# Optimization experiments

Hardware: AMD Instinct MI355X
Metric: run time of the kernel (lower is better)

The kernel has to match this reference:

```python
import jax, jax.numpy as jnp
import numpy as np

DIM = 384; EXP = 2; INNER = EXP * DIM            # 768
QKV_BS = 4
NH_Q = INNER // QKV_BS                            # 192 headwise-proj heads, head_dim 4
NH_M = QKV_BS                                     # 4 mLSTM heads
DH = INNER // NH_M                                # 192
B = 4; H = 32; W = 32; S = H * W                  # 1024 tokens
K = 3                                             # conv kernel
EPS = 1e-6


def setup_inputs() -> dict:
    key = jax.random.key(0)
    ks = jax.random.split(key, 16)
    def n(k, shape, scale):
        return jax.random.normal(k, shape, dtype=jnp.float32) * scale
    return {
        "x": jax.random.normal(ks[0], (B, S, DIM), dtype=jnp.float32),
        "W_up": n(ks[1], (2 * INNER, DIM), 0.02), "b_up": jnp.zeros((2 * INNER,), jnp.float32),
        "Wq": n(ks[2], (NH_Q, QKV_BS, QKV_BS), 0.1), "bq": jnp.zeros((INNER,), jnp.float32),
        "Wk": n(ks[3], (NH_Q, QKV_BS, QKV_BS), 0.1), "bk": jnp.zeros((INNER,), jnp.float32),
        "Wv": n(ks[4], (NH_Q, QKV_BS, QKV_BS), 0.1), "bv": jnp.zeros((INNER,), jnp.float32),
        "conv_w": n(ks[5], (K, K, 1, INNER), 0.1), "conv_b": jnp.zeros((INNER,), jnp.float32),
        "W_ig": n(ks[6], (NH_M, 3 * INNER), 0.01),
        "b_ig": jax.random.normal(ks[7], (NH_M,), dtype=jnp.float32) * 0.1 - 10.0,
        "W_fg": n(ks[8], (NH_M, 3 * INNER), 0.01),
        "b_fg": jnp.linspace(3.0, 6.0, NH_M, dtype=jnp.float32),
        "norm_w": jnp.ones((INNER,), jnp.float32), "norm_b": jnp.zeros((INNER,), jnp.float32),
        "skip": jnp.ones((INNER,), jnp.float32),
        "W_down": n(ks[9], (DIM, INNER), 0.02), "b_down": jnp.zeros((DIM,), jnp.float32),
    }


def _headwise(x, Wh, b):
    # block-diagonal linear: 192 independent 4x4 blocks
    Bx, Sx, _ = x.shape
    xh = x.reshape(Bx, Sx, NH_Q, QKV_BS)
    y = jnp.einsum('bshd,hod->bsho', xh, Wh)
    return y.reshape(Bx, Sx, INNER) + b


def reference(x, W_up, b_up, Wq, bq, Wk, bk, Wv, bv, conv_w, conv_b,
              W_ig, b_ig, W_fg, b_fg, norm_w, norm_b, skip, W_down, b_down):
    x_inner = x @ W_up.T + b_up                        # (B,S,2*INNER)
    x_m, z = jnp.split(x_inner, 2, axis=-1)
    # depthwise 2d conv over the (H,W) token grid
    img = x_m.reshape(B, H, W, INNER)
    conv = jax.lax.conv_general_dilated(
        img, conv_w, window_strides=(1, 1), padding='SAME',
        dimension_numbers=('NHWC', 'HWIO', 'NHWC'), feature_group_count=INNER)
    conv = (conv + conv_b).reshape(B, S, INNER)
    conv_act = jax.nn.silu(conv)
    q = _headwise(conv_act, Wq, bq)
    k = _headwise(conv_act, Wk, bk)
    v = _headwise(x_m, Wv, bv)
    # ---- mLSTM cell (parallel stabilized form) ----
    gate_in = jnp.concatenate([q, k, v], axis=-1)      # (B,S,3*INNER)
    ig = jnp.einsum('bsf,hf->bhs', gate_in, W_ig) + b_ig[None, :, None]   # (B,NH,S)
    fg = jnp.einsum('bsf,hf->bhs', gate_in, W_fg) + b_fg[None, :, None]
    qh = q.reshape(B, S, NH_M, DH).transpose(0, 2, 1, 3)                  # (B,NH,S,DH)
    kh = k.reshape(B, S, NH_M, DH).transpose(0, 2, 1, 3)
    vh = v.reshape(B, S, NH_M, DH).transpose(0, 2, 1, 3)
    log_f = jax.nn.log_sigmoid(fg)                     # (B,NH,S)
    lfc = jnp.cumsum(log_f, axis=-1)                   # cumulative log forget gates
    dmat = lfc[:, :, :, None] - lfc[:, :, None, :]     # [i,j] = lfc[i]-lfc[j]
    mask = jnp.tril(jnp.ones((S, S), dtype=bool))
    log_fg_mat = jnp.where(mask, dmat, -jnp.inf)
    log_D = log_fg_mat + ig[:, :, None, :]             # add input gate of column j
    max_log_D = jnp.max(log_D, axis=-1, keepdims=True)
    Dm = jnp.exp(log_D - max_log_D)
    qkT = jnp.einsum('bhsd,bhtd->bhst', qh, kh) / jnp.sqrt(jnp.float32(DH))
    C = qkT * Dm
    normalizer = jnp.maximum(jnp.abs(C.sum(-1, keepdims=True)), jnp.exp(-max_log_D))
    Cn = C / (normalizer + EPS)
    h = jnp.einsum('bhst,bhtd->bhsd', Cn, vh)          # (B,NH,S,DH)
    # multi-head layernorm over DH (group_norm with NH groups)
    mean = h.mean(-1, keepdims=True)
    var = h.var(-1, keepdims=True)
    hn = (h - mean) * jax.lax.rsqrt(var + 1e-5)
    hn = hn * norm_w.reshape(NH_M, DH)[None, :, None, :] + norm_b.reshape(NH_M, DH)[None, :, None, :]
    h_tilde = hn.transpose(0, 2, 1, 3).reshape(B, S, INNER)
    # ---- skip, output gating, down projection ----
    h_skip = h_tilde + skip * conv_act
    h_state = h_skip * jax.nn.silu(z)
    return h_state @ W_down.T + b_down
```

## Files before the change

### kernel.cpp

```cpp
#include <hip/hip_runtime.h>
#include <hip/hip_bf16.h>


#define B_     4
#define S_     1024
#define DIM_   384
#define INNER_ 768
#define NHM_   4
#define DH_    192
#define NTOK   (B_*S_)
#define SLOTS_ 40

typedef __attribute__((ext_vector_type(8))) __bf16 bf16x8v;
typedef __attribute__((ext_vector_type(4))) float  f32x4;

static __device__ __forceinline__ f32x4 mfma16(bf16x8v a, bf16x8v b, f32x4 c) {
  return __builtin_amdgcn_mfma_f32_16x16x32_bf16(a, b, c, 0, 0, 0);
}

__global__ __launch_bounds__(256) void cast_all_k(
    const float* __restrict__ x, const float* __restrict__ wup,
    const float* __restrict__ wdn,
    __hip_bfloat16* __restrict__ xb, __hip_bfloat16* __restrict__ wub,
    __hip_bfloat16* __restrict__ wdb)
{
  constexpr int N1 = NTOK * DIM_ / 4;
  constexpr int N2 = N1 + 1536 * DIM_ / 4;
  constexpr int N3 = N2 + DIM_ * INNER_ / 4;
  const int i = blockIdx.x * 256 + threadIdx.x;
  if (i >= N3) return;
  const float* src; __hip_bfloat16* dst; int j;
  if (i < N1)      { src = x;   dst = xb;  j = i; }
  else if (i < N2) { src = wup; dst = wub; j = i - N1; }
  else             { src = wdn; dst = wdb; j = i - N2; }
  const float4 v = *(const float4*)&src[(size_t)j * 4];
  dst[j * 4 + 0] = __float2bfloat16(v.x);
  dst[j * 4 + 1] = __float2bfloat16(v.y);
  dst[j * 4 + 2] = __float2bfloat16(v.z);
  dst[j * 4 + 3] = __float2bfloat16(v.w);
}

__global__ __launch_bounds__(256) void gemm_up_lds_k(
    const __hip_bfloat16* __restrict__ A,
    const __hip_bfloat16* __restrict__ Bw,
    const float* __restrict__ bias, float* __restrict__ xm,
    __hip_bfloat16* __restrict__ gz)
{
  constexpr int NSTEP = DIM_ / 64;
  __shared__ __hip_bfloat16 Al[2][4096];
  __shared__ __hip_bfloat16 Bl[2][4096];
  const int n0 = blockIdx.x * 64, m0 = blockIdx.y * 64;
  const int tid = threadIdx.x;
  const int wave = tid >> 6, lane = tid & 63;
  const int lrow = lane & 15, lgrp = lane >> 4;

  const int r0 = tid >> 2, g0 = tid & 3;
  bf16x8v areg[2], breg[2];
  auto sload = [&](int k0) {
    areg[0] = *(const bf16x8v*)&A[(size_t)(m0 + r0) * DIM_ + k0 + g0 * 8];
    breg[0] = *(const bf16x8v*)&Bw[(size_t)(n0 + r0) * DIM_ + k0 + g0 * 8];
    areg[1] = *(const bf16x8v*)&A[(size_t)(m0 + r0) * DIM_ + k0 + 32 + g0 * 8];
    breg[1] = *(const bf16x8v*)&Bw[(size_t)(n0 + r0) * DIM_ + k0 + 32 + g0 * 8];
  };
  auto swrite = [&](int buf) {
    *(bf16x8v*)&Al[buf][(size_t)tid * 8]         = areg[0];
    *(bf16x8v*)&Bl[buf][(size_t)tid * 8]         = breg[0];
    *(bf16x8v*)&Al[buf][(size_t)(tid + 256) * 8] = areg[1];
    *(bf16x8v*)&Bl[buf][(size_t)(tid + 256) * 8] = breg[1];
  };

  f32x4 acc[4];
  #pragma unroll
  for (int nt = 0; nt < 4; ++nt) acc[nt] = f32x4{0.f, 0.f, 0.f, 0.f};

  sload(0); swrite(0);
  __syncthreads();
  int cur = 0;
  for (int ks = 0; ks < NSTEP; ++ks) {
    const bool nxt = (ks + 1 < NSTEP);
    if (nxt) sload((ks + 1) * 64);
    #pragma unroll
    for (int kk = 0; kk < 2; ++kk) {
      const bf16x8v af = *(const bf16x8v*)
          &Al[cur][(size_t)(kk * 256 + (wave * 16 + lrow) * 4 + lgrp) * 8];
      #pragma unroll
      for (int nt = 0; nt < 4; ++nt) {
        const bf16x8v bf = *(const bf16x8v*)
            &Bl[cur][(size_t)(kk * 256 + (nt * 16 + lrow) * 4 + lgrp) * 8];
        acc[nt] = mfma16(af, bf, acc[nt]);
      }
    }
    if (nxt) swrite(cur ^ 1);
    __syncthreads();
    cur ^= 1;
  }

  const bool zside = (n0 >= INNER_);
  #pragma unroll
  for (int nt = 0; nt < 4; ++nt) {
    const int n = n0 + nt * 16 + lrow;
    const float bv = bias[n];
    #pragma unroll
    for (int r = 0; r < 4; ++r) {
      const int m = m0 + wave * 16 + lgrp * 4 + r;
      const float v = acc[nt][r] + bv;
      if (!zside) {
        xm[(size_t)m * INNER_ + n] = v;
      } else {
        gz[(size_t)m * INNER_ + (n - INNER_)] =
            __float2bfloat16(v / (1.f + __expf(-v)));
      }
    }
  }
}

template<int KD>
__global__ __launch_bounds__(256) void gemm_lds_k(
    const __hip_bfloat16* __restrict__ A, int lda,
    const __hip_bfloat16* __restrict__ Bw, int ldb,
    float* __restrict__ C, int ldc)
{
  constexpr int NSTEP = KD / 64;
  __shared__ __hip_bfloat16 Al[2][4096];
  __shared__ __hip_bfloat16 Bl[2][4096];
  const int n0 = blockIdx.x * 64, m0 = blockIdx.y * 64;
  const int kofs = blockIdx.z * KD;
  const int tid = threadIdx.x;
  const int wave = tid >> 6, lane = tid & 63;
  const int lrow = lane & 15, lgrp = lane >> 4;

  const __hip_bfloat16* Ap = A + kofs;
  const __hip_bfloat16* Bp = Bw + kofs;
  float* Cp = C + (size_t)blockIdx.z * NTOK * ldc;

  const int r0 = tid >> 2, g0 = tid & 3;
  bf16x8v areg[2], breg[2];
  auto sload = [&](int k0) {
    areg[0] = *(const bf16x8v*)&Ap[(size_t)(m0 + r0) * lda + k0 + g0 * 8];
    breg[0] = *(const bf16x8v*)&Bp[(size_t)(n0 + r0) * ldb + k0 + g0 * 8];
    areg[1] = *(const bf16x8v*)&Ap[(size_t)(m0 + r0) * lda + k0 + 32 + g0 * 8];
    breg[1] = *(const bf16x8v*)&Bp[(size_t)(n0 + r0) * ldb + k0 + 32 + g0 * 8];
  };
  auto swrite = [&](int buf) {
    *(bf16x8v*)&Al[buf][(size_t)tid * 8]         = areg[0];
    *(bf16x8v*)&Bl[buf][(size_t)tid * 8]         = breg[0];
    *(bf16x8v*)&Al[buf][(size_t)(tid + 256) * 8] = areg[1];
    *(bf16x8v*)&Bl[buf][(size_t)(tid + 256) * 8] = breg[1];
  };

  f32x4 acc[4];
  #pragma unroll
  for (int nt = 0; nt < 4; ++nt) acc[nt] = f32x4{0.f, 0.f, 0.f, 0.f};

  sload(0); swrite(0);
  __syncthreads();
  int cur = 0;
  for (int ks = 0; ks < NSTEP; ++ks) {
    const bool nxt = (ks + 1 < NSTEP);
    if (nxt) sload((ks + 1) * 64);
    #pragma unroll
    for (int kk = 0; kk < 2; ++kk) {
      const bf16x8v af = *(const bf16x8v*)
          &Al[cur][(size_t)(kk * 256 + (wave * 16 + lrow) * 4 + lgrp) * 8];
      #pragma unroll
      for (int nt = 0; nt < 4; ++nt) {
        const bf16x8v bf = *(const bf16x8v*)
            &Bl[cur][(size_t)(kk * 256 + (nt * 16 + lrow) * 4 + lgrp) * 8];
        acc[nt] = mfma16(af, bf, acc[nt]);
      }
    }
    if (nxt) swrite(cur ^ 1);
    __syncthreads();
    cur ^= 1;
  }

  #pragma unroll
  for (int nt = 0; nt < 4; ++nt) {
    const int n = n0 + nt * 16 + lrow;
    #pragma unroll
    for (int r = 0; r < 4; ++r) {
      const int m = m0 + wave * 16 + lgrp * 4 + r;
      Cp[(size_t)m * ldc + n] = acc[nt][r];
    }
  }
}

__global__ __launch_bounds__(256) void gemm_down_red_k(
    const float* __restrict__ pws, const float* __restrict__ bias,
    float* __restrict__ out)
{
  const int i = blockIdx.x * 256 + threadIdx.x;
  if (i >= NTOK * DIM_ / 4) return;
  const int n4 = (i % (DIM_ / 4)) * 4;
  const float4 bv = *(const float4*)&bias[n4];
  float4 s0 = *(const float4*)&pws[(size_t)i * 4];
  const float4 s1 = *(const float4*)&pws[(size_t)NTOK * DIM_ + (size_t)i * 4];
  s0.x += s1.x + bv.x;
  s0.y += s1.y + bv.y;
  s0.z += s1.z + bv.z;
  s0.w += s1.w + bv.w;
  *(float4*)&out[(size_t)i * 4] = s0;
}

__global__ __launch_bounds__(256) void conv_headwise_k(
    const float* __restrict__ xm, const float* __restrict__ cw,
    const float* __restrict__ cb, __hip_bfloat16* __restrict__ cab,
    const float* __restrict__ Wq, const float* __restrict__ bq,
    const float* __restrict__ Wk, const float* __restrict__ bk,
    const float* __restrict__ Wv, const float* __restrict__ bv,
    const float* __restrict__ Wig, const float* __restrict__ big,
    const float* __restrict__ Wfg, const float* __restrict__ bfg,
    __hip_bfloat16* __restrict__ qbf, __hip_bfloat16* __restrict__ kbf,
    __hip_bfloat16* __restrict__ vbf,
    float* __restrict__ ig, float* __restrict__ fg)
{
  __shared__ float cas[INNER_], qs[INNER_], ks[INNER_], vs[INNER_];
  const int t = blockIdx.x;
  const int b = t >> 10, s = t & 1023;
  const int y = s >> 5, x = s & 31;
  const int tb = t - s;
  const int tid = threadIdx.x;

  if (tid < 192) {
    const int c4 = tid * 4;
    float4 acc = *(const float4*)&cb[c4];
    #pragma unroll
    for (int ky = -1; ky <= 1; ++ky) {
      const int yy = y + ky;
      if (yy < 0 || yy > 31) continue;
      #pragma unroll
      for (int kx = -1; kx <= 1; ++kx) {
        const int xx = x + kx;
        if (xx < 0 || xx > 31) continue;
        const float4 v = *(const float4*)&xm[(size_t)(tb + (yy << 5) + xx) * INNER_ + c4];
        const float4 w = *(const float4*)&cw[((ky + 1) * 3 + (kx + 1)) * INNER_ + c4];
        acc.x += v.x * w.x; acc.y += v.y * w.y;
        acc.z += v.z * w.z; acc.w += v.w * w.w;
      }
    }
    float4 o;
    o.x = acc.x / (1.f + __expf(-acc.x));
    o.y = acc.y / (1.f + __expf(-acc.y));
    o.z = acc.z / (1.f + __expf(-acc.z));
    o.w = acc.w / (1.f + __expf(-acc.w));
    *(float4*)&cas[c4] = o;
    __hip_bfloat16 tc[4] = {__float2bfloat16(o.x), __float2bfloat16(o.y),
                            __float2bfloat16(o.z), __float2bfloat16(o.w)};
    *(uint2*)&cab[(size_t)t * INNER_ + c4] = *(uint2*)tc;
  }
  __syncthreads();

  if (tid < 192) {
    const float4 cav4 = *(const float4*)&cas[tid * 4];
    const float4 xmv4 = *(const float4*)&xm[(size_t)t * INNER_ + tid * 4];
    const float cav[4] = {cav4.x, cav4.y, cav4.z, cav4.w};
    const float xmv[4] = {xmv4.x, xmv4.y, xmv4.z, xmv4.w};
    __hip_bfloat16 tq[4], tk[4], tv[4];
    #pragma unroll
    for (int o = 0; o < 4; ++o) {
      const int cidx = tid * 4 + o;
      float q = bq[cidx], k = bk[cidx], v = bv[cidx];
      #pragma unroll
      for (int d = 0; d < 4; ++d) {
        q += cav[d] * Wq[tid * 16 + o * 4 + d];
        k += cav[d] * Wk[tid * 16 + o * 4 + d];
        v += xmv[d] * Wv[tid * 16 + o * 4 + d];
      }
      qs[cidx] = q; ks[cidx] = k; vs[cidx] = v;
      tq[o] = __float2bfloat16(q);
      tk[o] = __float2bfloat16(k);
      tv[o] = __float2bfloat16(v);
    }
    const int cidx0 = tid * 4;
    const int hm = cidx0 / DH_, dd = cidx0 % DH_;
    const size_t o2 = ((size_t)(b * NHM_ + hm) * S_ + s) * DH_ + dd;
    *(uint2*)&qbf[o2] = *(uint2*)tq;
    *(uint2*)&kbf[o2] = *(uint2*)tk;
    *(uint2*)&vbf[o2] = *(uint2*)tv;
  }
  __syncthreads();

  const int g = tid >> 5, l32 = tid & 31;
  const float* Wg = (g < 4) ? Wig : Wfg;
  const int h = g & 3;
  float sum = 0.f;
  #pragma unroll
  for (int i = 0; i < 6; ++i) {
    const int c4 = (l32 + i * 32) * 4;
    const float4 qv = *(const float4*)&qs[c4];
    const float4 kv = *(const float4*)&ks[c4];
    const float4 vv = *(const float4*)&vs[c4];
    const float4 wq = *(const float4*)&Wg[h * 2304 + c4];
    const float4 wk = *(const float4*)&Wg[h * 2304 + 768 + c4];
    const float4 wv = *(const float4*)&Wg[h * 2304 + 1536 + c4];
    sum += qv.x * wq.x + qv.y * wq.y + qv.z * wq.z + qv.w * wq.w;
    sum += kv.x * wk.x + kv.y * wk.y + kv.z * wk.z + kv.w * wk.w;
    sum += vv.x * wv.x + vv.y * wv.y + vv.z * wv.z + vv.w * wv.w;
  }
  #pragma unroll
  for (int m = 16; m >= 1; m >>= 1) sum += __shfl_xor(sum, m);
  if (l32 == 0) {
    if (g < 4) ig[(size_t)(b * NHM_ + h) * S_ + s] = sum + big[h];
    else       fg[(size_t)(b * NHM_ + h) * S_ + s] = sum + bfg[h];
  }
}

__global__ __launch_bounds__(256) void aux_k(
    const __hip_bfloat16* __restrict__ vbf, __hip_bfloat16* __restrict__ vtb,
    const float* __restrict__ ig, const float* __restrict__ fg,
    float* __restrict__ lfc, float* __restrict__ aa, float* __restrict__ rm)
{
  const int blk = blockIdx.x;
  if (blk < 768) {
    __shared__ __hip_bfloat16 tile[64][72];
    const int s0 = (blk & 15) * 64;
    const int d0 = ((blk >> 4) % 3) * 64;
    const int bh = blk / 48;
    const int tid = threadIdx.x;
    const int rr = tid >> 3;
    const int cc8 = (tid & 7) * 8;
    #pragma unroll
    for (int it = 0; it < 2; ++it) {
      const int r = rr + it * 32;
      *(bf16x8v*)&tile[r][cc8] =
          *(const bf16x8v*)&vbf[((size_t)bh * S_ + s0 + r) * DH_ + d0 + cc8];
    }
    __syncthreads();
    #pragma unroll
    for (int it = 0; it < 2; ++it) {
      const int r = rr + it * 32;
      bf16x8v tmp;
      #pragma unroll
      for (int e = 0; e < 8; ++e) tmp[e] = *(__bf16*)&tile[cc8 + e][r];
      *(bf16x8v*)&vtb[((size_t)bh * DH_ + d0 + r) * S_ + s0 + cc8] = tmp;
    }
    return;
  }
  if (threadIdx.x >= 64) return;
  const int bh = blk - 768;
  const int lane = threadIdx.x;
  const float* fgp = fg + bh * S_;
  const float* igp = ig + bh * S_;
  float v[16];
  float run = 0.f;
  #pragma unroll
  for (int i = 0; i < 16; ++i) {
    const float xv = fgp[lane * 16 + i];
    const float lf = fminf(xv, 0.f) - log1pf(expf(-fabsf(xv)));
    run += lf;
    v[i] = run;
  }
  float inc = run;
  #pragma unroll
  for (int off = 1; off < 64; off <<= 1) {
    const float o = __shfl_up(inc, off);
    if (lane >= off) inc += o;
  }
  const float excl = inc - run;
  float rv[16];
  float rmx = -INFINITY;
  #pragma unroll
  for (int i = 0; i < 16; ++i) {
    const float l = v[i] + excl;
    lfc[bh * S_ + lane * 16 + i] = l;
    const float a = igp[lane * 16 + i] - l;
    aa[bh * S_ + lane * 16 + i] = a;
    rmx = fmaxf(rmx, a);
    rv[i] = rmx;
  }
  float incm = rmx;
  #pragma unroll
  for (int off = 1; off < 64; off <<= 1) {
    const float o = __shfl_up(incm, off);
    if (lane >= off) incm = fmaxf(incm, o);
  }
  float exm = __shfl_up(incm, 1);
  if (lane == 0) exm = -INFINITY;
  #pragma unroll
  for (int i = 0; i < 16; ++i) {
    rm[bh * S_ + lane * 16 + i] = fmaxf(rv[i], exm);
  }
}

__global__ __launch_bounds__(256) void mlstm_part_k(
    const __hip_bfloat16* __restrict__ qbf, const __hip_bfloat16* __restrict__ kbf,
    const __hip_bfloat16* __restrict__ vtb,
    const float* __restrict__ aa, const float* __restrict__ rm,
    float* __restrict__ pacc, float* __restrict__ rsp)
{
  __shared__ __hip_bfloat16 Kl[2][6144];
  __shared__ __hip_bfloat16 Vl[2][6144];
  __shared__ __hip_bfloat16 Pl[4][16][40];
  const int bh = blockIdx.x;
  const int slot = blockIdx.y;
  int t = 0, base = 0;
  #pragma unroll
  for (int s = 0; s < 16; ++s) {
    const int sz = (s >> 2) + 1;
    if (slot >= base + sz) { base += sz; t = s + 1; }
  }
  const int c = slot - base;
  const int jt_lo = c * 8;
  const int jt_hi = min(jt_lo + 8, 2 * t + 2);

  const int wave = threadIdx.x >> 6, lane = threadIdx.x & 63;
  const int lrow = lane & 15, lgrp = lane >> 4;
  const int q0 = t * 64 + wave * 16;
  const __hip_bfloat16* Q  = qbf + (size_t)bh * S_ * DH_;
  const __hip_bfloat16* Kp = kbf + (size_t)bh * S_ * DH_;
  const __hip_bfloat16* VT = vtb + (size_t)bh * DH_ * S_;
  const float* aap = aa + bh * S_;
  const float* rmp = rm + bh * S_;

  bf16x8v qf[6];
  #pragma unroll
  for (int kk = 0; kk < 6; ++kk)
    qf[kk] = *(const bf16x8v*)&Q[(size_t)(q0 + lrow) * DH_ + kk * 32 + lgrp * 8];
  float rmi[4];
  #pragma unroll
  for (int r = 0; r < 4; ++r) rmi[r] = rmp[q0 + lgrp * 4 + r];

  const f32x4 zero4 = {0.f, 0.f, 0.f, 0.f};
  f32x4 hacc[12];
  #pragma unroll
  for (int dd = 0; dd < 12; ++dd) hacc[dd] = zero4;
  float rs[4] = {0.f, 0.f, 0.f, 0.f};
  const float scale = 0.07216878364870323f;
  const int myqmax = q0 + 15;

  bf16x8v kreg[3], vreg[3];
  const int s0_ = wave * 192 + lane;

  auto stage_load = [&](int j0s) {
    #pragma unroll
    for (int i = 0; i < 3; ++i) {
      const int s = s0_ + i * 64;
      const int kk = s >> 7, jr = (s >> 2) & 31, g = s & 3;
      kreg[i] = *(const bf16x8v*)&Kp[(size_t)(j0s + jr) * DH_ + kk * 32 + g * 8];
      const int d = s >> 2;
      vreg[i] = *(const bf16x8v*)&VT[(size_t)d * S_ + j0s + g * 8];
    }
  };
  auto stage_write = [&](int buf) {
    #pragma unroll
    for (int i = 0; i < 3; ++i) {
      const int s = s0_ + i * 64;
      *(bf16x8v*)&Kl[buf][s << 3] = kreg[i];
      *(bf16x8v*)&Vl[buf][s << 3] = vreg[i];
    }
  };

  stage_load(jt_lo * 32);
  stage_write(0);
  __syncthreads();
  int cur = 0;

  for (int jt = jt_lo; jt < jt_hi; ++jt) {
    const int j0 = jt * 32;
    const bool nxt = (jt + 1 < jt_hi);
    if (nxt) stage_load((jt + 1) * 32);
    if (j0 <= myqmax) {
      f32x4 sacc[2];
      sacc[0] = zero4; sacc[1] = zero4;
      #pragma unroll
      for (int jj = 0; jj < 2; ++jj) {
        #pragma unroll
        for (int kk = 0; kk < 6; ++kk) {
          const bf16x8v kf = *(const bf16x8v*)
              &Kl[cur][(kk * 128 + (jj * 16 + lrow) * 4 + lgrp) << 3];
          sacc[jj] = mfma16(qf[kk], kf, sacc[jj]);
        }
      }
      #pragma unroll
      for (int jj = 0; jj < 2; ++jj) {
        const int j = j0 + jj * 16 + lrow;
        const float ajv = aap[j];
        #pragma unroll
        for (int r = 0; r < 4; ++r) {
          const int i_ = q0 + lgrp * 4 + r;
          float cval = 0.f;
          if (j <= i_) cval = sacc[jj][r] * scale * __expf(ajv - rmi[r]);
          rs[r] += cval;
          Pl[wave][lgrp * 4 + r][jj * 16 + lrow] = __float2bfloat16(cval);
        }
      }
      const bf16x8v pf = *(const bf16x8v*)&Pl[wave][lrow][lgrp * 8];
      #pragma unroll
      for (int dd = 0; dd < 12; ++dd) {
        const bf16x8v vf = *(const bf16x8v*)
            &Vl[cur][(dd * 64 + lrow * 4 + lgrp) << 3];
        hacc[dd] = mfma16(pf, vf, hacc[dd]);
      }
    }
    if (nxt) stage_write(cur ^ 1);
    __syncthreads();
    cur ^= 1;
  }

  #pragma unroll
  for (int r = 0; r < 4; ++r) {
    #pragma unroll
    for (int m = 1; m < 16; m <<= 1) rs[r] += __shfl_xor(rs[r], m);
  }
  const size_t pb16 = ((size_t)bh * SLOTS_ + slot) * 16 + wave * 4 + lgrp;
  #pragma unroll
  for (int dd = 0; dd < 12; ++dd) {
    *(f32x4*)&pacc[(pb16 * 12 + dd) * 64 + lrow * 4] = hacc[dd];
  }
  if (lrow == 0) {
    #pragma unroll
    for (int r = 0; r < 4; ++r)
      rsp[((size_t)bh * SLOTS_ + slot) * 64 + wave * 16 + lgrp * 4 + r] = rs[r];
  }
}

__global__ __launch_bounds__(256) void mlstm_red_k(
    const float* __restrict__ pacc, const float* __restrict__ rsp,
    const float* __restrict__ lfc, const float* __restrict__ rm,
    const __hip_bfloat16* __restrict__ cab, const __hip_bfloat16* __restrict__ gz,
    const float* __restrict__ nw, const float* __restrict__ nb,
    const float* __restrict__ skip, __hip_bfloat16* __restrict__ hs)
{
  const int t = blockIdx.x, bh = blockIdx.y;
  const int b = bh >> 2, hm = bh & 3;
  int base = 0;
  #pragma unroll
  for (int s = 0; s < 16; ++s) if (s < t) base += (s >> 2) + 1;
  const int nc = (t >> 2) + 1;

  const int wave = threadIdx.x >> 6, lane = threadIdx.x & 63;
  const int lrow = lane & 15, lgrp = lane >> 4;
  const int q0 = t * 64 + wave * 16;
  const float* lfcp = lfc + bh * S_;
  const float* rmp  = rm + bh * S_;

  f32x4 hsum[12];
  #pragma unroll
  for (int dd = 0; dd < 12; ++dd) hsum[dd] = f32x4{0.f, 0.f, 0.f, 0.f};
  float rst[4] = {0.f, 0.f, 0.f, 0.f};

  for (int cc = 0; cc < nc; ++cc) {
    const size_t pb16 = ((size_t)bh * SLOTS_ + base + cc) * 16 + wave * 4 + lgrp;
    #pragma unroll
    for (int dd = 0; dd < 12; ++dd) {
      const f32x4 p = *(const f32x4*)&pacc[(pb16 * 12 + dd) * 64 + lrow * 4];
      hsum[dd] += p;
    }
    #pragma unroll
    for (int r = 0; r < 4; ++r)
      rst[r] += rsp[((size_t)bh * SLOTS_ + base + cc) * 64 + wave * 16 + lgrp * 4 + r];
  }

  #pragma unroll
  for (int r = 0; r < 4; ++r) {
    const int i_ = q0 + lgrp * 4 + r;
    const int tok = b * S_ + i_;
    const float mld = lfcp[i_] + rmp[i_];
    const float nrm = fmaxf(fabsf(rst[r]), __expf(-mld)) + 1e-6f;
    float hv[12];
    float sum = 0.f, sq = 0.f;
    #pragma unroll
    for (int dd = 0; dd < 12; ++dd) {
      const float x = hsum[dd][r] / nrm;
      hv[dd] = x; sum += x; sq += x * x;
    }
    #pragma unroll
    for (int m = 1; m < 16; m <<= 1) {
      sum += __shfl_xor(sum, m);
      sq  += __shfl_xor(sq, m);
    }
    const float mean = sum * (1.f / 192.f);
    const float var  = sq * (1.f / 192.f) - mean * mean;
    const float rstd = rsqrtf(var + 1e-5f);
    #pragma unroll
    for (int dd = 0; dd < 12; ++dd) {
      const int cidx = hm * DH_ + dd * 16 + lrow;
      const float hn = (hv[dd] - mean) * rstd * nw[cidx] + nb[cidx];
      const float cav = __bfloat162float(cab[(size_t)tok * INNER_ + cidx]);
      const float gzv = __bfloat162float(gz[(size_t)tok * INNER_ + cidx]);
      const float hsv = (hn + skip[cidx] * cav) * gzv;
      hs[(size_t)tok * INNER_ + cidx] = __float2bfloat16(hsv);
    }
  }
}

extern "C" void kernel_launch(void* const* d_in, const int* in_sizes, int n_in,
                              void* d_out, int out_size, void* d_ws, size_t ws_size,
                              hipStream_t stream) {
  const float* x      = (const float*)d_in[0];
  const float* W_up   = (const float*)d_in[1];
  const float* b_up   = (const float*)d_in[2];
  const float* Wq     = (const float*)d_in[3];
  const float* bq     = (const float*)d_in[4];
  const float* Wk     = (const float*)d_in[5];
  const float* bk     = (const float*)d_in[6];
  const float* Wv     = (const float*)d_in[7];
  const float* bv     = (const float*)d_in[8];
  const float* conv_w = (const float*)d_in[9];
  const float* conv_b = (const float*)d_in[10];
  const float* W_ig   = (const float*)d_in[11];
  const float* b_ig   = (const float*)d_in[12];
  const float* W_fg   = (const float*)d_in[13];
  const float* b_fg   = (const float*)d_in[14];
  const float* norm_w = (const float*)d_in[15];
  const float* norm_b = (const float*)d_in[16];
  const float* skip   = (const float*)d_in[17];
  const float* W_down = (const float*)d_in[18];
  const float* b_down = (const float*)d_in[19];
  float* out = (float*)d_out;

  char* ws = (char*)d_ws;
  constexpr size_t OFF_XM  = 0;
  constexpr size_t OFF_GZ  = OFF_XM + (size_t)NTOK * INNER_ * 4;
  constexpr size_t OFF_CA  = OFF_GZ + (size_t)NTOK * INNER_ * 2;
  constexpr size_t OFF_QBF = OFF_CA + (size_t)NTOK * INNER_ * 2;
  constexpr size_t OFF_KBF = OFF_QBF + (size_t)16 * S_ * DH_ * 2;
  constexpr size_t OFF_VBF = OFF_KBF + (size_t)16 * S_ * DH_ * 2;
  constexpr size_t OFF_IG  = OFF_VBF + (size_t)16 * S_ * DH_ * 2;
  constexpr size_t OFF_FG  = OFF_IG + (size_t)16 * S_ * 4;
  constexpr size_t OFF_LFC = OFF_FG + (size_t)16 * S_ * 4;
  constexpr size_t OFF_AA  = OFF_LFC + (size_t)16 * S_ * 4;
  constexpr size_t OFF_RM  = OFF_AA + (size_t)16 * S_ * 4;
  constexpr size_t OFF_HS  = OFF_RM + (size_t)16 * S_ * 4;
  constexpr size_t OFF_XB  = OFF_HS + (size_t)NTOK * INNER_ * 2;
  constexpr size_t OFF_WUB = OFF_XB + (size_t)NTOK * DIM_ * 2;
  constexpr size_t OFF_WDB = OFF_WUB + (size_t)1536 * DIM_ * 2;
  constexpr size_t OFF_VTB = OFF_WDB + (size_t)DIM_ * INNER_ * 2;
  constexpr size_t OFF_PAC = OFF_VTB + (size_t)16 * DH_ * S_ * 2;
  constexpr size_t OFF_RSP = OFF_PAC + (size_t)16 * SLOTS_ * 64 * 192 * 4;

  float* xm  = (float*)(ws + OFF_XM);
  __hip_bfloat16* gz  = (__hip_bfloat16*)(ws + OFF_GZ);
  __hip_bfloat16* cab = (__hip_bfloat16*)(ws + OFF_CA);
  __hip_bfloat16* qbf = (__hip_bfloat16*)(ws + OFF_QBF);
  __hip_bfloat16* kbf = (__hip_bfloat16*)(ws + OFF_KBF);
  __hip_bfloat16* vbf = (__hip_bfloat16*)(ws + OFF_VBF);
  float* ig  = (float*)(ws + OFF_IG);
  float* fg  = (float*)(ws + OFF_FG);
  float* lfc = (float*)(ws + OFF_LFC);
  float* aav = (float*)(ws + OFF_AA);
  float* rmv = (float*)(ws + OFF_RM);
  __hip_bfloat16* hsb = (__hip_bfloat16*)(ws + OFF_HS);
  __hip_bfloat16* xb  = (__hip_bfloat16*)(ws + OFF_XB);
  __hip_bfloat16* wub = (__hip_bfloat16*)(ws + OFF_WUB);
  __hip_bfloat16* wdb = (__hip_bfloat16*)(ws + OFF_WDB);
  __hip_bfloat16* vtb = (__hip_bfloat16*)(ws + OFF_VTB);
  float* pacc = (float*)(ws + OFF_PAC);
  float* rsp  = (float*)(ws + OFF_RSP);
  float* pws  = pacc;

  {
    constexpr int N3 = NTOK * DIM_ / 4 + 1536 * DIM_ / 4 + DIM_ * INNER_ / 4;
    cast_all_k<<<(N3 + 255) / 256, 256, 0, stream>>>(x, W_up, W_down, xb, wub, wdb);
  }
  gemm_up_lds_k<<<dim3(24, 64), 256, 0, stream>>>(xb, wub, b_up, xm, gz);
  conv_headwise_k<<<NTOK, 256, 0, stream>>>(
      xm, conv_w, conv_b, cab,
      Wq, bq, Wk, bk, Wv, bv, W_ig, b_ig, W_fg, b_fg,
      qbf, kbf, vbf, ig, fg);
  aux_k<<<784, 256, 0, stream>>>(vbf, vtb, ig, fg, lfc, aav, rmv);
  mlstm_part_k<<<dim3(16, SLOTS_), 256, 0, stream>>>(qbf, kbf, vtb, aav, rmv, pacc, rsp);
  mlstm_red_k<<<dim3(16, 16), 256, 0, stream>>>(
      pacc, rsp, lfc, rmv, cab, gz, norm_w, norm_b, skip, hsb);
  gemm_lds_k<DIM_><<<dim3(6, 64, 2), 256, 0, stream>>>(
      hsb, INNER_, wdb, INNER_, pws, DIM_);
  gemm_down_red_k<<<(NTOK * DIM_ / 4 + 255) / 256, 256, 0, stream>>>(pws, b_down, out);
}
```

Before: 119.6 us.

## Store mLSTM partials in bf16 and drop split-K for down projection

```diff
diff --git a/kernel.cpp b/kernel.cpp
--- a/kernel.cpp
+++ b/kernel.cpp
@@ -118,28 +118,23 @@
 __global__ __launch_bounds__(256) void gemm_lds_k(
     const __hip_bfloat16* __restrict__ A, int lda,
     const __hip_bfloat16* __restrict__ Bw, int ldb,
-    float* __restrict__ C, int ldc)
+    const float* __restrict__ bias, float* __restrict__ C, int ldc)
 {
   constexpr int NSTEP = KD / 64;
   __shared__ __hip_bfloat16 Al[2][4096];
   __shared__ __hip_bfloat16 Bl[2][4096];
   const int n0 = blockIdx.x * 64, m0 = blockIdx.y * 64;
-  const int kofs = blockIdx.z * KD;
   const int tid = threadIdx.x;
   const int wave = tid >> 6, lane = tid & 63;
   const int lrow = lane & 15, lgrp = lane >> 4;
 
-  const __hip_bfloat16* Ap = A + kofs;
-  const __hip_bfloat16* Bp = Bw + kofs;
-  float* Cp = C + (size_t)blockIdx.z * NTOK * ldc;
-
   const int r0 = tid >> 2, g0 = tid & 3;
   bf16x8v areg[2], breg[2];
   auto sload = [&](int k0) {
-    areg[0] = *(const bf16x8v*)&Ap[(size_t)(m0 + r0) * lda + k0 + g0 * 8];
-    breg[0] = *(const bf16x8v*)&Bp[(size_t)(n0 + r0) * ldb + k0 + g0 * 8];
-    areg[1] = *(const bf16x8v*)&Ap[(size_t)(m0 + r0) * lda + k0 + 32 + g0 * 8];
-    breg[1] = *(const bf16x8v*)&Bp[(size_t)(n0 + r0) * ldb + k0 + 32 + g0 * 8];
+    areg[0] = *(const bf16x8v*)&A[(size_t)(m0 + r0) * lda + k0 + g0 * 8];
+    breg[0] = *(const bf16x8v*)&Bw[(size_t)(n0 + r0) * ldb + k0 + g0 * 8];
+    areg[1] = *(const bf16x8v*)&A[(size_t)(m0 + r0) * lda + k0 + 32 + g0 * 8];
+    breg[1] = *(const bf16x8v*)&Bw[(size_t)(n0 + r0) * ldb + k0 + 32 + g0 * 8];
   };
   auto swrite = [&](int buf) {
     *(bf16x8v*)&Al[buf][(size_t)tid * 8]         = areg[0];
@@ -177,29 +172,13 @@
   #pragma unroll
   for (int nt = 0; nt < 4; ++nt) {
     const int n = n0 + nt * 16 + lrow;
+    const float bv = bias[n];
     #pragma unroll
     for (int r = 0; r < 4; ++r) {
       const int m = m0 + wave * 16 + lgrp * 4 + r;
-      Cp[(size_t)m * ldc + n] = acc[nt][r];
-    }
-  }
-}
-
-__global__ __launch_bounds__(256) void gemm_down_red_k(
-    const float* __restrict__ pws, const float* __restrict__ bias,
-    float* __restrict__ out)
-{
-  const int i = blockIdx.x * 256 + threadIdx.x;
-  if (i >= NTOK * DIM_ / 4) return;
-  const int n4 = (i % (DIM_ / 4)) * 4;
-  const float4 bv = *(const float4*)&bias[n4];
-  float4 s0 = *(const float4*)&pws[(size_t)i * 4];
-  const float4 s1 = *(const float4*)&pws[(size_t)NTOK * DIM_ + (size_t)i * 4];
-  s0.x += s1.x + bv.x;
-  s0.y += s1.y + bv.y;
-  s0.z += s1.z + bv.z;
-  s0.w += s1.w + bv.w;
-  *(float4*)&out[(size_t)i * 4] = s0;
+      C[(size_t)m * ldc + n] = acc[nt][r] + bv;
+    }
+  }
 }
 
 __global__ __launch_bounds__(256) void conv_headwise_k(
@@ -386,7 +365,7 @@
     const __hip_bfloat16* __restrict__ qbf, const __hip_bfloat16* __restrict__ kbf,
     const __hip_bfloat16* __restrict__ vtb,
     const float* __restrict__ aa, const float* __restrict__ rm,
-    float* __restrict__ pacc, float* __restrict__ rsp)
+    __hip_bfloat16* __restrict__ pacc, float* __restrict__ rsp)
 {
   __shared__ __hip_bfloat16 Kl[2][6144];
   __shared__ __hip_bfloat16 Vl[2][6144];
@@ -505,7 +484,11 @@
   const size_t pb16 = ((size_t)bh * SLOTS_ + slot) * 16 + wave * 4 + lgrp;
   #pragma unroll
   for (int dd = 0; dd < 12; ++dd) {
-    *(f32x4*)&pacc[(pb16 * 12 + dd) * 64 + lrow * 4] = hacc[dd];
+    __hip_bfloat16 tp[4] = {__float2bfloat16(hacc[dd][0]),
+                            __float2bfloat16(hacc[dd][1]),
+                            __float2bfloat16(hacc[dd][2]),
+                            __float2bfloat16(hacc[dd][3])};
+    *(uint2*)&pacc[(pb16 * 12 + dd) * 64 + lrow * 4] = *(uint2*)tp;
   }
   if (lrow == 0) {
     #pragma unroll
@@ -515,7 +498,7 @@
 }
 
 __global__ __launch_bounds__(256) void mlstm_red_k(
-    const float* __restrict__ pacc, const float* __restrict__ rsp,
+    const __hip_bfloat16* __restrict__ pacc, const float* __restrict__ rsp,
     const float* __restrict__ lfc, const float* __restrict__ rm,
     const __hip_bfloat16* __restrict__ cab, const __hip_bfloat16* __restrict__ gz,
     const float* __restrict__ nw, const float* __restrict__ nb,
@@ -543,8 +526,12 @@
     const size_t pb16 = ((size_t)bh * SLOTS_ + base + cc) * 16 + wave * 4 + lgrp;
     #pragma unroll
     for (int dd = 0; dd < 12; ++dd) {
-      const f32x4 p = *(const f32x4*)&pacc[(pb16 * 12 + dd) * 64 + lrow * 4];
-      hsum[dd] += p;
+      const uint2 pv = *(const uint2*)&pacc[(pb16 * 12 + dd) * 64 + lrow * 4];
+      const __hip_bfloat16* pb = (const __hip_bfloat16*)&pv;
+      hsum[dd][0] += __bfloat162float(pb[0]);
+      hsum[dd][1] += __bfloat162float(pb[1]);
+      hsum[dd][2] += __bfloat162float(pb[2]);
+      hsum[dd][3] += __bfloat162float(pb[3]);
     }
     #pragma unroll
     for (int r = 0; r < 4; ++r)
@@ -627,7 +614,7 @@
   constexpr size_t OFF_WDB = OFF_WUB + (size_t)1536 * DIM_ * 2;
   constexpr size_t OFF_VTB = OFF_WDB + (size_t)DIM_ * INNER_ * 2;
   constexpr size_t OFF_PAC = OFF_VTB + (size_t)16 * DH_ * S_ * 2;
-  constexpr size_t OFF_RSP = OFF_PAC + (size_t)16 * SLOTS_ * 64 * 192 * 4;
+  constexpr size_t OFF_RSP = OFF_PAC + (size_t)16 * SLOTS_ * 64 * 192 * 2;
 
   float* xm  = (float*)(ws + OFF_XM);
   __hip_bfloat16* gz  = (__hip_bfloat16*)(ws + OFF_GZ);
@@ -645,9 +632,8 @@
   __hip_bfloat16* wub = (__hip_bfloat16*)(ws + OFF_WUB);
   __hip_bfloat16* wdb = (__hip_bfloat16*)(ws + OFF_WDB);
   __hip_bfloat16* vtb = (__hip_bfloat16*)(ws + OFF_VTB);
-  float* pacc = (float*)(ws + OFF_PAC);
-  float* rsp  = (float*)(ws + OFF_RSP);
-  float* pws  = pacc;
+  __hip_bfloat16* pacc = (__hip_bfloat16*)(ws + OFF_PAC);
+  float* rsp = (float*)(ws + OFF_RSP);
 
   {
     constexpr int N3 = NTOK * DIM_ / 4 + 1536 * DIM_ / 4 + DIM_ * INNER_ / 4;
@@ -662,7 +648,6 @@
   mlstm_part_k<<<dim3(16, SLOTS_), 256, 0, stream>>>(qbf, kbf, vtb, aav, rmv, pacc, rsp);
   mlstm_red_k<<<dim3(16, 16), 256, 0, stream>>>(
       pacc, rsp, lfc, rmv, cab, gz, norm_w, norm_b, skip, hsb);
-  gemm_lds_k<DIM_><<<dim3(6, 64, 2), 256, 0, stream>>>(
-      hsb, INNER_, wdb, INNER_, pws, DIM_);
-  gemm_down_red_k<<<(NTOK * DIM_ / 4 + 255) / 256, 256, 0, stream>>>(pws, b_down, out);
-}
+  gemm_lds_k<INNER_><<<dim3(6, 64), 256, 0, stream>>>(
+      hsb, INNER_, wdb, INNER_, b_down, out, DIM_);
+}
```

After: 112.2 us, median of 2. -6.2%, faster.
